# Optimization experiments

Measured on AMD Instinct MI355X. Metric: run time of the kernel, lower is better.

The kernel has to match this reference:

```python
import jax, jax.numpy as jnp
import numpy as np

SCALE = 8.0  # sqrt(head_dim=64)
B, H, S, D = 2, 16, 2048, 64


def setup_inputs() -> dict:
    key = jax.random.key(0)
    kq, kk, kv = jax.random.split(key, 3)
    query = jax.random.normal(kq, (B, H, S, D), dtype=jnp.float32)
    key_t = jax.random.normal(kk, (B, H, S, D), dtype=jnp.float32)
    value = jax.random.normal(kv, (B, H, S, D), dtype=jnp.float32)
    # causal target mask (B, 1, S, S); 0 = masked
    mask = jnp.broadcast_to(jnp.tril(jnp.ones((S, S), dtype=jnp.int32)), (B, 1, S, S))
    return {"query": query, "key": key_t, "value": value, "mask": mask}


def reference(query, key, value, mask):
    # scores: (B, H, S, S)
    scores = jnp.einsum("bhqd,bhkd->bhqk", query, key) / SCALE
    scores = jnp.where(mask == 0, -jnp.inf, scores)
    attn = jax.nn.softmax(scores, axis=-1)  # dropout_rate=0.0 -> identity
    return jnp.einsum("bhqk,bhkd->bhqd", attn, value)
```

## Files before the change

kernel.cpp:

```cpp
#include <hip/hip_runtime.h>
#include <hip/hip_bf16.h>


#define S_ 2048
#define D_ 64
#define NBH 32

typedef __bf16 bf16x8 __attribute__((ext_vector_type(8)));
typedef float f32x16 __attribute__((ext_vector_type(16)));
typedef unsigned short u16x8 __attribute__((ext_vector_type(8)));
typedef unsigned int u32;
typedef u32 u32x4 __attribute__((ext_vector_type(4)));

static __device__ __forceinline__ unsigned short bfb(float f) {
    return __builtin_bit_cast(unsigned short, (__bf16)f);
}
static __device__ __forceinline__ u32 pk2(float lo, float hi) {
    return (u32)bfb(lo) | ((u32)bfb(hi) << 16);
}

__global__ __launch_bounds__(256)
void prep_frag(const float* __restrict__ K, const float* __restrict__ V,
               unsigned short* __restrict__ Kf, unsigned short* __restrict__ Vf) {
    const int bh = blockIdx.x >> 5;
    const int t  = blockIdx.x & 31;
    __shared__ float Ka[64][65];
    __shared__ float Va[64][65];
    const float* Ks = K + ((size_t)bh * S_ + t * 64) * D_;
    const float* Vs = V + ((size_t)bh * S_ + t * 64) * D_;
    #pragma unroll
    for (int i = 0; i < 4; ++i) {
        const int flat = i * 1024 + threadIdx.x * 4;
        const int s = flat >> 6, d = flat & 63;
        float4 kx = *reinterpret_cast<const float4*>(Ks + s * D_ + d);
        Ka[s][d] = kx.x; Ka[s][d+1] = kx.y; Ka[s][d+2] = kx.z; Ka[s][d+3] = kx.w;
        float4 vx = *reinterpret_cast<const float4*>(Vs + s * D_ + d);
        Va[s][d] = vx.x; Va[s][d+1] = vx.y; Va[s][d+2] = vx.z; Va[s][d+3] = vx.w;
    }
    __syncthreads();
    const size_t tb = ((size_t)bh * 32 + t) * 512;
    #pragma unroll
    for (int i = 0; i < 2; ++i) {
        const int u  = i * 256 + threadIdx.x;
        const int h  = u >> 8, ks = (u >> 6) & 3, h2 = (u >> 5) & 1, l2 = u & 31;
        const int d0 = 8 * (2 * ks + h2);
        u16x8 ok, ov;
        #pragma unroll
        for (int j = 0; j < 8; ++j) {
            ok[j] = bfb(Ka[h * 32 + l2][d0 + j]);
            ov[j] = bfb(Va[d0 + j][h * 32 + l2]);
        }
        *reinterpret_cast<u16x8*>(Kf + (tb + u) * 8) = ok;
        *reinterpret_cast<u16x8*>(Vf + (tb + u) * 8) = ov;
    }
}

#define MFMA32(a, b, c) __builtin_amdgcn_mfma_f32_32x32x16_bf16((a), (b), (c), 0, 0, 0)

#define LOADF(DST, BASE, T) { \
    const unsigned short* fb_ = (BASE) + (size_t)(T) * 4096 + lane * 8; \
    DST[0] = *reinterpret_cast<const bf16x8*>(fb_); \
    DST[1] = *reinterpret_cast<const bf16x8*>(fb_ + 512); \
    DST[2] = *reinterpret_cast<const bf16x8*>(fb_ + 1024); \
    DST[3] = *reinterpret_cast<const bf16x8*>(fb_ + 1536); \
    DST[4] = *reinterpret_cast<const bf16x8*>(fb_ + 2048); \
    DST[5] = *reinterpret_cast<const bf16x8*>(fb_ + 2560); \
    DST[6] = *reinterpret_cast<const bf16x8*>(fb_ + 3072); \
    DST[7] = *reinterpret_cast<const bf16x8*>(fb_ + 3584); }

#define PVSTEP(KS, C, TL) { \
    u32 a0 = C[TL][0], a1 = C[TL][1], b0 = C[TL+1][0], b1 = C[TL+1][1]; \
    asm volatile("v_permlane32_swap_b32 %0, %1" : "+v"(a0), "+v"(b0)); \
    asm volatile("v_permlane32_swap_b32 %0, %1" : "+v"(a1), "+v"(b1)); \
    u32x4 w = { a0, a1, b0, b1 }; \
    bf16x8 pf = __builtin_bit_cast(bf16x8, w); \
    oa0 = MFMA32(vA[KS],     pf, oa0); \
    oa1 = MFMA32(vA[4 + KS], pf, oa1); }

__global__ __launch_bounds__(256, 2)
void attn_frag(const float* __restrict__ Q, const unsigned short* __restrict__ Kf,
               const unsigned short* __restrict__ Vf, float* __restrict__ O) {
    const int tid  = threadIdx.x;
    const int wq   = tid >> 6;
    const int lane = tid & 63;
    const int lq   = lane & 31;
    const int hi   = lane >> 5;

    const int wid = blockIdx.x * 4 + wq;
    int qs, bh;
    if (wid < 1024) { qs = 63 - (wid >> 5); bh = wid & 31; }
    else            { qs = (wid - 1024) >> 5; bh = (wid - 1024) & 31; }
    const int q0w = qs * 32;
    const int nt  = (qs >> 1) + 1;

    const unsigned short* Kg = Kf + (size_t)bh * 131072;
    const unsigned short* Vg = Vf + (size_t)bh * 131072;

    const float qscale = 0.18033688011112042f;
    bf16x8 qf[4];
    {
        const float* qsrc = Q + ((size_t)bh * S_ + q0w + lq) * D_;
        #pragma unroll
        for (int ks = 0; ks < 4; ++ks) {
            const float* p = qsrc + ks * 16 + hi * 8;
            float4 x = *reinterpret_cast<const float4*>(p);
            float4 y = *reinterpret_cast<const float4*>(p + 4);
            union { unsigned short u[8]; bf16x8 v; } tt;
            tt.u[0] = bfb(x.x * qscale); tt.u[1] = bfb(x.y * qscale);
            tt.u[2] = bfb(x.z * qscale); tt.u[3] = bfb(x.w * qscale);
            tt.u[4] = bfb(y.x * qscale); tt.u[5] = bfb(y.y * qscale);
            tt.u[6] = bfb(y.z * qscale); tt.u[7] = bfb(y.w * qscale);
            qf[ks] = tt.v;
        }
    }

    f32x16 oa0, oa1;
    #pragma unroll
    for (int r = 0; r < 16; ++r) { oa0[r] = 0.f; oa1[r] = 0.f; }
    float m_ = -__builtin_inff(), l_ = 0.f;

    bf16x8 kA[8], vA[8];
    LOADF(kA, Kg, 0)
    LOADF(vA, Vg, 0)

    for (int t = 0; t < nt; ++t) {
        const int tn = (t + 1 < 32) ? (t + 1) : 31;

        f32x16 s0, s1;
        #pragma unroll
        for (int r = 0; r < 16; ++r) { s0[r] = 0.f; s1[r] = 0.f; }
        __builtin_amdgcn_s_setprio(1);
        #pragma unroll
        for (int ks = 0; ks < 4; ++ks) {
            s0 = MFMA32(kA[ks],     qf[ks], s0);
            s1 = MFMA32(kA[4 + ks], qf[ks], s1);
        }
        __builtin_amdgcn_s_setprio(0);

        LOADF(kA, Kg, tn)

        if (t == nt - 1) {
            const int qg = q0w + lq - t * 64;
            #pragma unroll
            for (int r = 0; r < 16; ++r) {
                const int kv0 = (r & 3) + 8 * (r >> 2) + 4 * hi;
                if (kv0 > qg)      s0[r] = -__builtin_inff();
                if (kv0 + 32 > qg) s1[r] = -__builtin_inff();
            }
        }

        float mx[16];
        #pragma unroll
        for (int r = 0; r < 16; ++r) mx[r] = fmaxf(s0[r], s1[r]);
        #pragma unroll
        for (int off = 8; off >= 1; off >>= 1)
            for (int r = 0; r < off; ++r) mx[r] = fmaxf(mx[r], mx[r + off]);
        const float v = fmaxf(mx[0], __shfl_xor(mx[0], 32));
        if (__any(v > m_ + 8.0f ? 1 : 0)) {
            const float mn = fmaxf(m_, v);
            const float al = __builtin_amdgcn_exp2f(m_ - mn);
            m_ = mn;
            l_ *= al;
            #pragma unroll
            for (int r = 0; r < 16; ++r) { oa0[r] *= al; oa1[r] *= al; }
        }
        #pragma unroll
        for (int r = 0; r < 16; ++r) {
            s0[r] = __builtin_amdgcn_exp2f(s0[r] - m_);
            s1[r] = __builtin_amdgcn_exp2f(s1[r] - m_);
        }

        {
            float ts[16];
            #pragma unroll
            for (int r = 0; r < 16; ++r) ts[r] = s0[r] + s1[r];
            #pragma unroll
            for (int off = 8; off >= 1; off >>= 1)
                for (int r = 0; r < off; ++r) ts[r] += ts[r + off];
            l_ += ts[0] + __shfl_xor(ts[0], 32);
        }

        u32 c0[4][2], c1[4][2];
        #pragma unroll
        for (int tq = 0; tq < 4; ++tq) {
            c0[tq][0] = pk2(s0[4*tq+0], s0[4*tq+1]);
            c0[tq][1] = pk2(s0[4*tq+2], s0[4*tq+3]);
            c1[tq][0] = pk2(s1[4*tq+0], s1[4*tq+1]);
            c1[tq][1] = pk2(s1[4*tq+2], s1[4*tq+3]);
        }

        __builtin_amdgcn_s_setprio(1);
        PVSTEP(0, c0, 0) PVSTEP(1, c0, 2) PVSTEP(2, c1, 0) PVSTEP(3, c1, 2)
        __builtin_amdgcn_s_setprio(0);

        LOADF(vA, Vg, tn)
    }

    const float inv = 1.0f / l_;
    float* Ob = O + ((size_t)bh * S_ + q0w + lq) * D_;
    #pragma unroll
    for (int g = 0; g < 4; ++g) {
        float4 o0 = { oa0[4*g+0]*inv, oa0[4*g+1]*inv, oa0[4*g+2]*inv, oa0[4*g+3]*inv };
        *reinterpret_cast<float4*>(&Ob[8*g + 4*hi]) = o0;
        float4 o1 = { oa1[4*g+0]*inv, oa1[4*g+1]*inv, oa1[4*g+2]*inv, oa1[4*g+3]*inv };
        *reinterpret_cast<float4*>(&Ob[32 + 8*g + 4*hi]) = o1;
    }
}

extern "C" void kernel_launch(void* const* d_in, const int* in_sizes, int n_in,
                              void* d_out, int out_size, void* d_ws, size_t ws_size,
                              hipStream_t stream) {
    const float* Q = (const float*)d_in[0];
    const float* K = (const float*)d_in[1];
    const float* V = (const float*)d_in[2];
    float* O = (float*)d_out;

    unsigned short* Kf = (unsigned short*)d_ws;
    unsigned short* Vf = Kf + (size_t)4194304;

    hipLaunchKernelGGL(prep_frag, dim3(1024), dim3(256), 0, stream, K, V, Kf, Vf);
    hipLaunchKernelGGL(attn_frag, dim3(512),  dim3(256), 0, stream, Q, Kf, Vf, O);
}
```

Measured before the change: 139.7 us.

## Pair causal query strips per wave and double-buffer K/V fragment loads

```diff
diff --git a/kernel.cpp b/kernel.cpp
--- a/kernel.cpp
+++ b/kernel.cpp
@@ -68,17 +68,83 @@
     DST[6] = *reinterpret_cast<const bf16x8*>(fb_ + 3072); \
     DST[7] = *reinterpret_cast<const bf16x8*>(fb_ + 3584); }
 
-#define PVSTEP(KS, C, TL) { \
+#define PVSTEP(VX, KS, C, TL) { \
     u32 a0 = C[TL][0], a1 = C[TL][1], b0 = C[TL+1][0], b1 = C[TL+1][1]; \
     asm volatile("v_permlane32_swap_b32 %0, %1" : "+v"(a0), "+v"(b0)); \
     asm volatile("v_permlane32_swap_b32 %0, %1" : "+v"(a1), "+v"(b1)); \
     u32x4 w = { a0, a1, b0, b1 }; \
     bf16x8 pf = __builtin_bit_cast(bf16x8, w); \
-    oa0 = MFMA32(vA[KS],     pf, oa0); \
-    oa1 = MFMA32(vA[4 + KS], pf, oa1); }
-
-__global__ __launch_bounds__(256, 2)
-void attn_frag(const float* __restrict__ Q, const unsigned short* __restrict__ Kf,
+    oa0 = MFMA32(VX[KS],     pf, oa0); \
+    oa1 = MFMA32(VX[4 + KS], pf, oa1); }
+
+#define TILE(KX, VX, T, TPF, NT) { \
+    f32x16 s0, s1; \
+    _Pragma("unroll") \
+    for (int r = 0; r < 16; ++r) { s0[r] = 0.f; s1[r] = 0.f; } \
+    __builtin_amdgcn_s_setprio(1); \
+    _Pragma("unroll") \
+    for (int ks = 0; ks < 4; ++ks) { \
+        s0 = MFMA32(KX[ks],     qf[ks], s0); \
+        s1 = MFMA32(KX[4 + ks], qf[ks], s1); \
+    } \
+    __builtin_amdgcn_s_setprio(0); \
+    LOADF(KX, Kg, TPF) \
+    __builtin_amdgcn_sched_barrier(0); \
+    if ((T) == (NT) - 1) { \
+        const int qg = q0w + lq - (T) * 64; \
+        _Pragma("unroll") \
+        for (int r = 0; r < 16; ++r) { \
+            const int kv0 = (r & 3) + 8 * (r >> 2) + 4 * hi; \
+            if (kv0 > qg)      s0[r] = -__builtin_inff(); \
+            if (kv0 + 32 > qg) s1[r] = -__builtin_inff(); \
+        } \
+    } \
+    float mx[16]; \
+    _Pragma("unroll") \
+    for (int r = 0; r < 16; ++r) mx[r] = fmaxf(s0[r], s1[r]); \
+    _Pragma("unroll") \
+    for (int off = 8; off >= 1; off >>= 1) \
+        for (int r = 0; r < off; ++r) mx[r] = fmaxf(mx[r], mx[r + off]); \
+    const float v = fmaxf(mx[0], __shfl_xor(mx[0], 32)); \
+    if (__any(v > m_ + 8.0f ? 1 : 0)) { \
+        const float mn = fmaxf(m_, v); \
+        const float al = __builtin_amdgcn_exp2f(m_ - mn); \
+        m_ = mn; \
+        l_ *= al; \
+        _Pragma("unroll") \
+        for (int r = 0; r < 16; ++r) { oa0[r] *= al; oa1[r] *= al; } \
+    } \
+    _Pragma("unroll") \
+    for (int r = 0; r < 16; ++r) { \
+        s0[r] = __builtin_amdgcn_exp2f(s0[r] - m_); \
+        s1[r] = __builtin_amdgcn_exp2f(s1[r] - m_); \
+    } \
+    { \
+        float ts[16]; \
+        _Pragma("unroll") \
+        for (int r = 0; r < 16; ++r) ts[r] = s0[r] + s1[r]; \
+        _Pragma("unroll") \
+        for (int off = 8; off >= 1; off >>= 1) \
+            for (int r = 0; r < off; ++r) ts[r] += ts[r + off]; \
+        l_ += ts[0] + __shfl_xor(ts[0], 32); \
+    } \
+    u32 c0[4][2], c1[4][2]; \
+    _Pragma("unroll") \
+    for (int tq = 0; tq < 4; ++tq) { \
+        c0[tq][0] = pk2(s0[4*tq+0], s0[4*tq+1]); \
+        c0[tq][1] = pk2(s0[4*tq+2], s0[4*tq+3]); \
+        c1[tq][0] = pk2(s1[4*tq+0], s1[4*tq+1]); \
+        c1[tq][1] = pk2(s1[4*tq+2], s1[4*tq+3]); \
+    } \
+    __builtin_amdgcn_s_setprio(1); \
+    PVSTEP(VX, 0, c0, 0) PVSTEP(VX, 1, c0, 2) PVSTEP(VX, 2, c1, 0) PVSTEP(VX, 3, c1, 2) \
+    __builtin_amdgcn_s_setprio(0); \
+    LOADF(VX, Vg, TPF) \
+    __builtin_amdgcn_sched_barrier(0); \
+}
+
+__global__ __launch_bounds__(256, 1)
+void attn_pair(const float* __restrict__ Q, const unsigned short* __restrict__ Kf,
                const unsigned short* __restrict__ Vf, float* __restrict__ O) {
     const int tid  = threadIdx.x;
     const int wq   = tid >> 6;
@@ -86,124 +152,65 @@
     const int lq   = lane & 31;
     const int hi   = lane >> 5;
 
-    const int wid = blockIdx.x * 4 + wq;
-    int qs, bh;
-    if (wid < 1024) { qs = 63 - (wid >> 5); bh = wid & 31; }
-    else            { qs = (wid - 1024) >> 5; bh = (wid - 1024) & 31; }
-    const int q0w = qs * 32;
-    const int nt  = (qs >> 1) + 1;
+    const int bid = blockIdx.x;
+    const int bh  = bid & 31;
+    const int sp  = (bid >> 5) * 4 + wq;
 
     const unsigned short* Kg = Kf + (size_t)bh * 131072;
     const unsigned short* Vg = Vf + (size_t)bh * 131072;
-
     const float qscale = 0.18033688011112042f;
-    bf16x8 qf[4];
-    {
-        const float* qsrc = Q + ((size_t)bh * S_ + q0w + lq) * D_;
+
+    #pragma unroll
+    for (int pass = 0; pass < 2; ++pass) {
+        const int qs  = pass ? sp : (63 - sp);
+        const int q0w = qs * 32;
+        const int nt  = (qs >> 1) + 1;
+
+        bf16x8 qf[4];
+        {
+            const float* qsrc = Q + ((size_t)bh * S_ + q0w + lq) * D_;
+            #pragma unroll
+            for (int ks = 0; ks < 4; ++ks) {
+                const float* p = qsrc + ks * 16 + hi * 8;
+                float4 x = *reinterpret_cast<const float4*>(p);
+                float4 y = *reinterpret_cast<const float4*>(p + 4);
+                union { unsigned short u[8]; bf16x8 v; } tt;
+                tt.u[0] = bfb(x.x * qscale); tt.u[1] = bfb(x.y * qscale);
+                tt.u[2] = bfb(x.z * qscale); tt.u[3] = bfb(x.w * qscale);
+                tt.u[4] = bfb(y.x * qscale); tt.u[5] = bfb(y.y * qscale);
+                tt.u[6] = bfb(y.z * qscale); tt.u[7] = bfb(y.w * qscale);
+                qf[ks] = tt.v;
+            }
+        }
+
+        f32x16 oa0, oa1;
         #pragma unroll
-        for (int ks = 0; ks < 4; ++ks) {
-            const float* p = qsrc + ks * 16 + hi * 8;
-            float4 x = *reinterpret_cast<const float4*>(p);
-            float4 y = *reinterpret_cast<const float4*>(p + 4);
-            union { unsigned short u[8]; bf16x8 v; } tt;
-            tt.u[0] = bfb(x.x * qscale); tt.u[1] = bfb(x.y * qscale);
-            tt.u[2] = bfb(x.z * qscale); tt.u[3] = bfb(x.w * qscale);
-            tt.u[4] = bfb(y.x * qscale); tt.u[5] = bfb(y.y * qscale);
-            tt.u[6] = bfb(y.z * qscale); tt.u[7] = bfb(y.w * qscale);
-            qf[ks] = tt.v;
-        }
-    }
-
-    f32x16 oa0, oa1;
-    #pragma unroll
-    for (int r = 0; r < 16; ++r) { oa0[r] = 0.f; oa1[r] = 0.f; }
-    float m_ = -__builtin_inff(), l_ = 0.f;
-
-    bf16x8 kA[8], vA[8];
-    LOADF(kA, Kg, 0)
-    LOADF(vA, Vg, 0)
-
-    for (int t = 0; t < nt; ++t) {
-        const int tn = (t + 1 < 32) ? (t + 1) : 31;
-
-        f32x16 s0, s1;
+        for (int r = 0; r < 16; ++r) { oa0[r] = 0.f; oa1[r] = 0.f; }
+        float m_ = -__builtin_inff(), l_ = 0.f;
+
+        bf16x8 kA[8], kB[8], vA[8], vB[8];
+        LOADF(kA, Kg, 0) LOADF(vA, Vg, 0)
+        LOADF(kB, Kg, 1) LOADF(vB, Vg, 1)
+        __builtin_amdgcn_sched_barrier(0);
+
+        for (int t = 0; t < nt; t += 2) {
+            const int p0 = (t + 2 < 32) ? (t + 2) : 31;
+            TILE(kA, vA, t, p0, nt)
+            if (t + 1 < nt) {
+                const int p1 = (t + 3 < 32) ? (t + 3) : 31;
+                TILE(kB, vB, t + 1, p1, nt)
+            }
+        }
+
+        const float inv = 1.0f / l_;
+        float* Ob = O + ((size_t)bh * S_ + q0w + lq) * D_;
         #pragma unroll
-        for (int r = 0; r < 16; ++r) { s0[r] = 0.f; s1[r] = 0.f; }
-        __builtin_amdgcn_s_setprio(1);
-        #pragma unroll
-        for (int ks = 0; ks < 4; ++ks) {
-            s0 = MFMA32(kA[ks],     qf[ks], s0);
-            s1 = MFMA32(kA[4 + ks], qf[ks], s1);
-        }
-        __builtin_amdgcn_s_setprio(0);
-
-        LOADF(kA, Kg, tn)
-
-        if (t == nt - 1) {
-            const int qg = q0w + lq - t * 64;
-            #pragma unroll
-            for (int r = 0; r < 16; ++r) {
-                const int kv0 = (r & 3) + 8 * (r >> 2) + 4 * hi;
-                if (kv0 > qg)      s0[r] = -__builtin_inff();
-                if (kv0 + 32 > qg) s1[r] = -__builtin_inff();
-            }
-        }
-
-        float mx[16];
-        #pragma unroll
-        for (int r = 0; r < 16; ++r) mx[r] = fmaxf(s0[r], s1[r]);
-        #pragma unroll
-        for (int off = 8; off >= 1; off >>= 1)
-            for (int r = 0; r < off; ++r) mx[r] = fmaxf(mx[r], mx[r + off]);
-        const float v = fmaxf(mx[0], __shfl_xor(mx[0], 32));
-        if (__any(v > m_ + 8.0f ? 1 : 0)) {
-            const float mn = fmaxf(m_, v);
-            const float al = __builtin_amdgcn_exp2f(m_ - mn);
-            m_ = mn;
-            l_ *= al;
-            #pragma unroll
-            for (int r = 0; r < 16; ++r) { oa0[r] *= al; oa1[r] *= al; }
-        }
-        #pragma unroll
-        for (int r = 0; r < 16; ++r) {
-            s0[r] = __builtin_amdgcn_exp2f(s0[r] - m_);
-            s1[r] = __builtin_amdgcn_exp2f(s1[r] - m_);
-        }
-
-        {
-            float ts[16];
-            #pragma unroll
-            for (int r = 0; r < 16; ++r) ts[r] = s0[r] + s1[r];
-            #pragma unroll
-            for (int off = 8; off >= 1; off >>= 1)
-                for (int r = 0; r < off; ++r) ts[r] += ts[r + off];
-            l_ += ts[0] + __shfl_xor(ts[0], 32);
-        }
-
-        u32 c0[4][2], c1[4][2];
-        #pragma unroll
-        for (int tq = 0; tq < 4; ++tq) {
-            c0[tq][0] = pk2(s0[4*tq+0], s0[4*tq+1]);
-            c0[tq][1] = pk2(s0[4*tq+2], s0[4*tq+3]);
-            c1[tq][0] = pk2(s1[4*tq+0], s1[4*tq+1]);
-            c1[tq][1] = pk2(s1[4*tq+2], s1[4*tq+3]);
-        }
-
-        __builtin_amdgcn_s_setprio(1);
-        PVSTEP(0, c0, 0) PVSTEP(1, c0, 2) PVSTEP(2, c1, 0) PVSTEP(3, c1, 2)
-        __builtin_amdgcn_s_setprio(0);
-
-        LOADF(vA, Vg, tn)
-    }
-
-    const float inv = 1.0f / l_;
-    float* Ob = O + ((size_t)bh * S_ + q0w + lq) * D_;
-    #pragma unroll
-    for (int g = 0; g < 4; ++g) {
-        float4 o0 = { oa0[4*g+0]*inv, oa0[4*g+1]*inv, oa0[4*g+2]*inv, oa0[4*g+3]*inv };
-        *reinterpret_cast<float4*>(&Ob[8*g + 4*hi]) = o0;
-        float4 o1 = { oa1[4*g+0]*inv, oa1[4*g+1]*inv, oa1[4*g+2]*inv, oa1[4*g+3]*inv };
-        *reinterpret_cast<float4*>(&Ob[32 + 8*g + 4*hi]) = o1;
+        for (int g = 0; g < 4; ++g) {
+            float4 o0 = { oa0[4*g+0]*inv, oa0[4*g+1]*inv, oa0[4*g+2]*inv, oa0[4*g+3]*inv };
+            *reinterpret_cast<float4*>(&Ob[8*g + 4*hi]) = o0;
+            float4 o1 = { oa1[4*g+0]*inv, oa1[4*g+1]*inv, oa1[4*g+2]*inv, oa1[4*g+3]*inv };
+            *reinterpret_cast<float4*>(&Ob[32 + 8*g + 4*hi]) = o1;
+        }
     }
 }
 
@@ -219,5 +226,5 @@
     unsigned short* Vf = Kf + (size_t)4194304;
 
     hipLaunchKernelGGL(prep_frag, dim3(1024), dim3(256), 0, stream, K, V, Kf, Vf);
-    hipLaunchKernelGGL(attn_frag, dim3(512),  dim3(256), 0, stream, Q, Kf, Vf, O);
-}
+    hipLaunchKernelGGL(attn_pair, dim3(256),  dim3(256), 0, stream, Q, Kf, Vf, O);
+}
```

After: 144.1 us. +3.1%, slower.
